# Optimization experiments

Hardware: AMD Instinct MI355X
Metric: run time of the kernel (lower is better)

The kernel has to match this reference:

```python
import jax, jax.numpy as jnp
import numpy as np

TOP_P = 0.9  # forward default arg, fixed to exercise the top-p path


def setup_inputs() -> dict:
    key = jax.random.key(0)
    k1, k2 = jax.random.split(key)
    B, V = 128, 128000
    logits = jax.random.normal(k1, (B, V), dtype=jnp.float32) * 2.0
    # temperatures in [0.5, 1.5) to avoid divide-by-near-zero
    temperatures = jax.random.uniform(k2, (B,), dtype=jnp.float32, minval=0.5, maxval=1.5)
    return {"logits": logits, "temperatures": temperatures, "top_k": 50}


def reference(logits, temperatures, top_k):
    B, V = logits.shape
    neg_inf = jnp.float32(-jnp.inf)

    # temperature scale + softmax
    scaled = logits.astype(jnp.float32) / temperatures[:, None]
    probs = jax.nn.softmax(scaled, axis=-1)  # (B, V)

    brow = jnp.arange(B)[:, None]

    # top-k filter: keep top-k probs, fill rest with -inf (matches torch scatter into full(-inf))
    if top_k > 0:
        k = min(top_k, V)
        vals, idx = jax.lax.top_k(probs, k)  # (B, k)
        probs = jnp.full_like(probs, neg_inf).at[brow, idx].set(vals)

    # top-p (nucleus) filter: sort desc, cumsum, mask tail beyond top_p (always keep first)
    if TOP_P < 1.0:
        order = jnp.argsort(-probs, axis=-1)              # descending order indices (-inf sorts last)
        sorted_probs = jnp.take_along_axis(probs, order, axis=-1)
        cum = jnp.cumsum(sorted_probs, axis=-1)
        remove = cum > TOP_P
        remove = remove.at[:, 0].set(False)
        sorted_probs = jnp.where(remove, neg_inf, sorted_probs)
        probs = probs.at[brow, order].set(sorted_probs)   # scatter back to original positions

    # Gumbel-max-style sampling: argmax(probs / Exp(1) noise), noise clamped to >= 1e-10
    kn = jax.random.fold_in(jax.random.key(0), 1)
    noise = jnp.maximum(jax.random.exponential(kn, probs.shape, dtype=jnp.float32), 1e-10)
    return jnp.argmax(probs / noise, axis=-1)  # (B,) int tokens
```

## Files before the change

### kernel.cpp

```cpp
#include <hip/hip_runtime.h>
#include <stdint.h>
#include <limits.h>

#define THREEFRY_PARTITIONABLE 1

#define NTK   512
#define NWAVE (NTK/64)
#define NBUCK 4096
#define BPT   (NBUCK/NTK)
#define CAPS  256
#define CAPG  2048
#define CAPF  512
#define KMAX  512
#define SMAX  32
#define CHUNK_TARGET 16384

#define NT1   1024
#define CAP1  4096

#if __has_builtin(__builtin_amdgcn_exp2f)
#define FAST_EXP2(x) __builtin_amdgcn_exp2f(x)
#else
#define FAST_EXP2(x) exp2f(x)
#endif

__device__ __forceinline__ uint32_t rotl32(uint32_t v, int r) {
  return (v << r) | (v >> (32 - r));
}
__device__ __forceinline__ void tfround(uint32_t& x0, uint32_t& x1, int r) {
  x0 += x1; x1 = rotl32(x1, r); x1 ^= x0;
}
__device__ __forceinline__ void threefry2x32(uint32_t k0, uint32_t k1,
                                             uint32_t x0, uint32_t x1,
                                             uint32_t& o0, uint32_t& o1) {
  uint32_t k2 = k0 ^ k1 ^ 0x1BD11BDAu;
  x0 += k0; x1 += k1;
  tfround(x0,x1,13); tfround(x0,x1,15); tfround(x0,x1,26); tfround(x0,x1,6);
  x0 += k1; x1 += k2 + 1u;
  tfround(x0,x1,17); tfround(x0,x1,29); tfround(x0,x1,16); tfround(x0,x1,24);
  x0 += k2; x1 += k0 + 2u;
  tfround(x0,x1,13); tfround(x0,x1,15); tfround(x0,x1,26); tfround(x0,x1,6);
  x0 += k0; x1 += k1 + 3u;
  tfround(x0,x1,17); tfround(x0,x1,29); tfround(x0,x1,16); tfround(x0,x1,24);
  x0 += k1; x1 += k2 + 4u;
  tfround(x0,x1,13); tfround(x0,x1,15); tfround(x0,x1,26); tfround(x0,x1,6);
  x0 += k2; x1 += k0 + 5u;
  o0 = x0; o1 = x1;
}
__device__ __forceinline__ float jax_noise(uint32_t kn0, uint32_t kn1,
                                           unsigned long long i,
                                           unsigned long long total) {
  uint32_t o0, o1, bits;
#if THREEFRY_PARTITIONABLE
  threefry2x32(kn0, kn1, (uint32_t)(i >> 32), (uint32_t)(i & 0xFFFFFFFFull), o0, o1);
  bits = o0 ^ o1;
#else
  unsigned long long H = total >> 1;
  if (i < H) { threefry2x32(kn0, kn1, (uint32_t)i, (uint32_t)(i + H), o0, o1); bits = o0; }
  else       { threefry2x32(kn0, kn1, (uint32_t)(i - H), (uint32_t)i, o0, o1); bits = o1; }
#endif
  float u = __uint_as_float((bits >> 9) | 0x3f800000u) - 1.0f;
  float e = -log1pf(-u);
  return fmaxf(e, 1e-10f);
}
__device__ __forceinline__ uint32_t fkey(float f) {
  uint32_t u = __float_as_uint(f);
  return u ^ ((u >> 31) ? 0xFFFFFFFFu : 0x80000000u);
}
__device__ __forceinline__ float unfkey_floor(uint32_t keyT) {
  if (keyT == 0u) return -INFINITY;
  return __uint_as_float((keyT & 0x80000000u) ? (keyT ^ 0x80000000u) : ~keyT);
}
__device__ __forceinline__ int clamp_k(int k) {
  if (k < 1) k = 1;
  if (k > KMAX) k = KMAX;
  return k;
}

__device__ __forceinline__ void block_kth_bucket(uint32_t* hist, uint32_t* wtot,
                                                 int* beta_sh, int k,
                                                 int tid, int lane, int wave) {
  const int base = tid * BPT;
  uint32_t tsum = 0;
#pragma unroll
  for (int j = 0; j < BPT; j++) tsum += hist[base + j];
  uint32_t incl = tsum;
  for (int off = 1; off < 64; off <<= 1) {
    uint32_t v = __shfl_down(incl, off);
    if (lane + off < 64) incl += v;
  }
  if (lane == 0) wtot[wave] = incl;
  __syncthreads();
  uint32_t above = incl - tsum;
  for (int w = wave + 1; w < NWAVE; w++) above += wtot[w];
  if (above < (uint32_t)k && above + tsum >= (uint32_t)k) {
    uint32_t run = above;
    for (int j = BPT - 1; j >= 0; j--) {
      run += hist[base + j];
      if (run >= (uint32_t)k) { *beta_sh = base + j; break; }
    }
  }
  __syncthreads();
}

__global__ __launch_bounds__(NTK)
void sampler_stream(const float* __restrict__ logits,
                    const float* __restrict__ temps,
                    const int* __restrict__ topk_ptr,
                    float* __restrict__ msArr,
                    double* __restrict__ dsumArr,
                    int* __restrict__ cntArr,
                    float2* __restrict__ pairs,
                    int B, int V, int S, int chunk) {
  const int blk = blockIdx.x;
  const int b = blk / S, sp = blk % S;
  const int tid = threadIdx.x, lane = tid & 63, wave = tid >> 6;

  __shared__ uint32_t hist[NBUCK];
  __shared__ float wm[NWAVE];
  __shared__ double wsum[NWAVE];
  __shared__ uint32_t wtot[NWAVE];
  __shared__ int beta_sh, cnum_sh;

  if (tid == 0) { beta_sh = 0; cnum_sh = 0; }
  for (int i = tid; i < NBUCK; i += NTK) hist[i] = 0;

  const float T = temps[b];
  const float cf = (float)(1.4426950408889634 / (double)T);
  const int k = clamp_k(*topk_ptr);

  const int start = sp * chunk;
  const int end = min(start + chunk, V);
  const float* row = logits + (size_t)b * (size_t)V;
  const int n = (end > start) ? (end - start) : 0;
  const int n4 = n >> 2;
  const float4* row4 = (const float4*)(row + start);

  float v0 = -INFINITY, v1 = -INFINITY;
  int   i0 = 0, i1 = 0;
  float acc0 = 0.f, acc1 = 0.f;

  auto proc = [&](float f, int idx) {
    bool gt0 = f > v0;
    bool gt1 = f > v1;
    float nv1 = gt0 ? v0 : (gt1 ? f : v1);
    int   ni1 = gt0 ? i0 : (gt1 ? idx : i1);
    v1 = nv1; i1 = ni1;
    v0 = gt0 ? f : v0;
    i0 = gt0 ? idx : i0;
  };
  auto proc4 = [&](float4 f, int vb) {
    proc(f.x, vb); proc(f.y, vb + 1); proc(f.z, vb + 2); proc(f.w, vb + 3);
    acc0 += FAST_EXP2(f.x * cf) + FAST_EXP2(f.z * cf);
    acc1 += FAST_EXP2(f.y * cf) + FAST_EXP2(f.w * cf);
  };

  int i = tid;
  for (; i + 3 * NTK < n4; i += 4 * NTK) {
    float4 fa = row4[i];
    float4 fb = row4[i + NTK];
    float4 fc = row4[i + 2 * NTK];
    float4 fd = row4[i + 3 * NTK];
    proc4(fa, start + i * 4);
    proc4(fb, start + (i + NTK) * 4);
    proc4(fc, start + (i + 2 * NTK) * 4);
    proc4(fd, start + (i + 3 * NTK) * 4);
  }
  for (; i < n4; i += NTK) {
    float4 fa = row4[i];
    proc4(fa, start + i * 4);
  }
  for (int v = start + n4 * 4 + tid; v < end; v += NTK) {
    float f = row[v];
    proc(f, v);
    acc0 += FAST_EXP2(f * cf);
  }

  float bm = v0;
  for (int off = 32; off; off >>= 1)
    bm = fmaxf(bm, __shfl_down(bm, off));
  if (lane == 0) wm[wave] = bm;

  double ds = (double)acc0 + (double)acc1;
  for (int off = 32; off; off >>= 1)
    ds += __shfl_down(ds, off);
  if (lane == 0) wsum[wave] = ds;

  if (v0 != -INFINITY) atomicAdd(&hist[fkey(v0) >> 20], 1u);
  __syncthreads();

  if (tid == 0) {
    float m_sp = wm[0];
#pragma unroll
    for (int w = 1; w < NWAVE; w++) m_sp = fmaxf(m_sp, wm[w]);
    msArr[blk] = m_sp;
    double t = 0.0;
    for (int w = 0; w < NWAVE; w++) t += wsum[w];
    dsumArr[blk] = t;
  }

  block_kth_bucket(hist, wtot, &beta_sh, k, tid, lane, wave);

  const float fT = unfkey_floor((uint32_t)beta_sh << 20);
  float2* myp = pairs + (size_t)blk * CAPS;

  if (v0 >= fT) {
    if (v1 >= fT) {
      for (int i2 = tid; i2 < n4; i2 += NTK) {
        float4 f = row4[i2];
        const int vb = start + i2 * 4;
        if (f.x >= fT) { int p = atomicAdd(&cnum_sh, 1); if (p < CAPS) myp[p] = make_float2(f.x, __int_as_float(vb)); }
        if (f.y >= fT) { int p = atomicAdd(&cnum_sh, 1); if (p < CAPS) myp[p] = make_float2(f.y, __int_as_float(vb + 1)); }
        if (f.z >= fT) { int p = atomicAdd(&cnum_sh, 1); if (p < CAPS) myp[p] = make_float2(f.z, __int_as_float(vb + 2)); }
        if (f.w >= fT) { int p = atomicAdd(&cnum_sh, 1); if (p < CAPS) myp[p] = make_float2(f.w, __int_as_float(vb + 3)); }
      }
      for (int v = start + n4 * 4 + tid; v < end; v += NTK) {
        float f = row[v];
        if (f >= fT) { int p = atomicAdd(&cnum_sh, 1); if (p < CAPS) myp[p] = make_float2(f, __int_as_float(v)); }
      }
    } else {
      int p = atomicAdd(&cnum_sh, 1);
      if (p < CAPS) myp[p] = make_float2(v0, __int_as_float(i0));
    }
  }
  __syncthreads();
  if (tid == 0) cntArr[blk] = min(cnum_sh, CAPS);
}

__global__ __launch_bounds__(NTK)
void sampler_finalize(const float* __restrict__ temps,
                      const int* __restrict__ topk_ptr,
                      const float* __restrict__ msArr,
                      const double* __restrict__ dsumArr,
                      const int* __restrict__ cntArr,
                      const float2* __restrict__ pairs,
                      int* __restrict__ out,
                      int B, int V, int S) {
  const int b = blockIdx.x;
  const int tid = threadIdx.x, lane = tid & 63, wave = tid >> 6;

  __shared__ uint32_t hist[NBUCK];
  __shared__ float gv[CAPG];
  __shared__ int   gi[CAPG];
  __shared__ float c2v[CAPF];
  __shared__ int   c2i[CAPF];
  __shared__ float c2p[CAPF];
  __shared__ float sv[KMAX];
  __shared__ int   si[KMAX];
  __shared__ float sc[KMAX];
  __shared__ int   offL[SMAX + 1];
  __shared__ int   cnL[SMAX];
  __shared__ float msL[SMAX];
  __shared__ double dsL[SMAX];
  __shared__ uint32_t wtot[NWAVE];
  __shared__ int beta_sh, cnt2_sh, L_sh;
  __shared__ float m_sh, D_sh;

  const int k = clamp_k(*topk_ptr);
  const float T = temps[b];

  if (tid == 0) { beta_sh = 0; cnt2_sh = 0; }
  if (tid < S) {
    msL[tid] = msArr[b * S + tid];
    dsL[tid] = dsumArr[b * S + tid];
    int c = cntArr[b * S + tid];
    cnL[tid] = (c < CAPS) ? c : CAPS;
  }
  for (int i = tid; i < NBUCK; i += NTK) hist[i] = 0;
  __syncthreads();

  if (tid == 0) {
    int acc = 0;
    for (int j = 0; j < S; j++) { offL[j] = acc; acc += cnL[j]; }
    offL[S] = acc;
  }

  if (wave == 1 || (NWAVE == 1 && wave == 0)) {
    float msp = (lane < S) ? msL[lane] : -INFINITY;
    float mg = msp;
    for (int off = 32; off; off >>= 1)
      mg = fmaxf(mg, __shfl_down(mg, off));
    mg = __shfl(mg, 0);
    double term = (lane < S) ? dsL[lane] : 0.0;
    for (int off = 32; off; off >>= 1)
      term += __shfl_down(term, off);
    if (lane == 0) {
      const double cd = 1.4426950408889634 / (double)T;
      D_sh = (float)(term * exp2(-(double)mg * cd));
      m_sh = mg / T;
    }
  }
  __syncthreads();

  const int TC = min(offL[S], CAPG);

  for (int t = tid; t < TC; t += NTK) {
    int j = 0;
#pragma unroll
    for (int jj = 1; jj <= SMAX; jj++)
      if (jj <= S) j += (t >= offL[jj]);
    float2 pr = pairs[(size_t)(b * S + j) * CAPS + (t - offL[j])];
    gv[t] = pr.x;
    gi[t] = __float_as_int(pr.y);
    atomicAdd(&hist[fkey(pr.x) >> 20], 1u);
  }
  __syncthreads();

  block_kth_bucket(hist, wtot, &beta_sh, k, tid, lane, wave);

  const float fT = unfkey_floor((uint32_t)beta_sh << 20);
  for (int t = tid; t < TC; t += NTK) {
    float val = gv[t];
    if (val >= fT) {
      int pos = atomicAdd(&cnt2_sh, 1);
      if (pos < CAPF) { c2v[pos] = val; c2i[pos] = gi[t]; }
    }
  }
  __syncthreads();

  const int C = min(cnt2_sh, CAPF);
  const float m = m_sh, D = D_sh;
  for (int i = tid; i < C; i += NTK)
    c2p[i] = expf(c2v[i] / T - m) / D;
  __syncthreads();

  for (int i = tid; i < C; i += NTK) {
    float pi = c2p[i];
    int   ii = c2i[i];
    int r = 0;
    for (int j = 0; j < C; j++) {
      float pj = c2p[j];
      r += (pj > pi) || (pj == pi && c2i[j] < ii);
    }
    if (r < k) { sv[r] = pi; si[r] = ii; }
  }
  __syncthreads();

  const int kk = (k < C) ? k : C;
  if (tid == 0) {
    float cum = 0.f;
    int L = 1;
    for (int j = 0; j < kk; j++) {
      cum += sv[j];
      if (j == 0) continue;
      if (cum <= 0.9f) L = j + 1; else break;
    }
    L_sh = L;
  }
  __syncthreads();

  const int L = L_sh;
  {
    uint32_t kn0, kn1;
    threefry2x32(0u, 0u, 0u, 1u, kn0, kn1);
    unsigned long long total = (unsigned long long)B * (unsigned long long)V;
    for (int j = tid; j < L; j += NTK) {
      unsigned long long flat = (unsigned long long)b * (unsigned long long)V
                              + (unsigned long long)si[j];
      sc[j] = sv[j] / jax_noise(kn0, kn1, flat, total);
    }
  }
  __syncthreads();

  if (tid == 0) {
    float bs = -1.0f;
    int   bi = INT_MAX;
    for (int j = 0; j < L; j++) {
      if (sc[j] > bs || (sc[j] == bs && si[j] < bi)) { bs = sc[j]; bi = si[j]; }
    }
    out[b] = bi;
  }
}

__global__ __launch_bounds__(NT1, 1)
void sampler_fallback(const float* __restrict__ logits,
                      const float* __restrict__ temps,
                      const int* __restrict__ topk_ptr,
                      int* __restrict__ out,
                      int B, int V) {
  const int b    = blockIdx.x;
  const int tid  = threadIdx.x;
  const int lane = tid & 63;
  const int wave = tid >> 6;

  __shared__ uint32_t hist[NBUCK];
  __shared__ float    cand_p[CAP1];
  __shared__ int      cand_i[CAP1];
  __shared__ float    wmax[16];
  __shared__ double   wsum[16];
  __shared__ float    svals[KMAX];
  __shared__ int      sidx[KMAX];
  __shared__ float    m_sh, D_sh;
  __shared__ int      beta_sh, cnum_sh, L_sh;

  const float T = temps[b];
  const float* row = logits + (size_t)b * (size_t)V;
  int k = clamp_k(*topk_ptr);
  if (k > V) k = V;

  if (tid == 0) { beta_sh = 1; cnum_sh = 0; }
  for (int i = tid; i < NBUCK; i += NT1) hist[i] = 0;
  __syncthreads();

  float t8[8];
#pragma unroll
  for (int j = 0; j < 8; j++) t8[j] = -INFINITY;
  float mymax = -INFINITY;
  for (int v = tid; v < V; v += NT1) {
    float s = row[v] / T;
    mymax = fmaxf(mymax, s);
    if (s > t8[0]) {
      t8[0] = s;
#pragma unroll
      for (int j = 1; j < 8; j++)
        if (t8[j-1] > t8[j]) { float tmp = t8[j]; t8[j] = t8[j-1]; t8[j-1] = tmp; }
    }
  }
  for (int off = 32; off > 0; off >>= 1)
    mymax = fmaxf(mymax, __shfl_down(mymax, off));
  if (lane == 0) wmax[wave] = mymax;
#pragma unroll
  for (int j = 0; j < 8; j++)
    if (t8[j] != -INFINITY) atomicAdd(&hist[fkey(t8[j]) >> 20], 1u);
  __syncthreads();
  if (tid == 0) {
    float m = -INFINITY;
    for (int w = 0; w < 16; w++) m = fmaxf(m, wmax[w]);
    m_sh = m;
  }
  if (wave == 1) {
    int base = lane * 64;
    uint32_t ssum = 0;
    for (int j = 0; j < 64; j++) ssum += hist[base + ((j + lane) & 63)];
    uint32_t incl = ssum;
    for (int off = 1; off < 64; off <<= 1) {
      uint32_t vv = __shfl_down(incl, off);
      if (lane + off < 64) incl += vv;
    }
    uint32_t higher = incl - ssum;
    if (higher < (uint32_t)k && incl >= (uint32_t)k) {
      uint32_t run = higher;
      for (int j = 63; j >= 0; j--) {
        run += hist[base + j];
        if (run >= (uint32_t)k) { beta_sh = base + j; break; }
      }
    }
  }
  __syncthreads();
  const float m = m_sh;
  const uint32_t keyT = (uint32_t)((beta_sh >= 1 ? beta_sh - 1 : 0)) << 20;
  double dsum = 0.0;
  for (int v = tid; v < V; v += NT1) {
    float s = row[v] / T;
    float e = expf(s - m);
    dsum += (double)e;
    if (fkey(s) >= keyT) {
      int pos = atomicAdd(&cnum_sh, 1);
      if (pos < CAP1) { cand_p[pos] = e; cand_i[pos] = v; }
    }
  }
  for (int off = 32; off > 0; off >>= 1)
    dsum += __shfl_down(dsum, off);
  if (lane == 0) wsum[wave] = dsum;
  __syncthreads();
  if (tid == 0) {
    double t = 0.0;
    for (int w = 0; w < 16; w++) t += wsum[w];
    D_sh = (float)t;
  }
  __syncthreads();
  const float D = D_sh;
  const int C = (cnum_sh < CAP1) ? cnum_sh : CAP1;
  for (int i = tid; i < C; i += NT1) cand_p[i] = cand_p[i] / D;
  __syncthreads();
  for (int i = tid; i < C; i += NT1) {
    float pi = cand_p[i];
    int   ii = cand_i[i];
    int r = 0;
    for (int j = 0; j < C; j++) {
      float pj = cand_p[j];
      r += (pj > pi) || (pj == pi && cand_i[j] < ii);
    }
    if (r < k) { svals[r] = pi; sidx[r] = ii; }
  }
  __syncthreads();
  if (tid == 0) {
    float cum = 0.f;
    int L = 1;
    for (int j = 0; j < k; j++) {
      cum += svals[j];
      if (j == 0) continue;
      if (cum <= 0.9f) L = j + 1; else break;
    }
    L_sh = L;
  }
  __syncthreads();
  const int L = L_sh;
  if (tid < L) {
    uint32_t kn0, kn1;
    threefry2x32(0u, 0u, 0u, 1u, kn0, kn1);
    unsigned long long total = (unsigned long long)B * (unsigned long long)V;
    unsigned long long flat = (unsigned long long)b * (unsigned long long)V
                            + (unsigned long long)sidx[tid];
    cand_p[tid] = svals[tid] / jax_noise(kn0, kn1, flat, total);
  }
  __syncthreads();
  if (tid == 0) {
    float bs = -1.0f;
    int   bi = INT_MAX;
    for (int j = 0; j < L; j++) {
      if (cand_p[j] > bs || (cand_p[j] == bs && sidx[j] < bi)) { bs = cand_p[j]; bi = sidx[j]; }
    }
    out[b] = bi;
  }
}

extern "C" void kernel_launch(void* const* d_in, const int* in_sizes, int n_in,
                              void* d_out, int out_size, void* d_ws, size_t ws_size,
                              hipStream_t stream) {
  const float* logits = (const float*)d_in[0];
  const float* temps  = (const float*)d_in[1];
  const int*   topk   = (const int*)d_in[2];
  int* out = (int*)d_out;

  int B = in_sizes[1];
  int V = in_sizes[0] / B;

  int S = (V + CHUNK_TARGET - 1) / CHUNK_TARGET;
  if (S > SMAX) S = SMAX;
  if (S < 1) S = 1;
  size_t need;
  for (;;) {
    need = (size_t)B * S * (sizeof(double) + sizeof(float) + sizeof(int))
         + (size_t)B * S * CAPS * sizeof(float2);
    if (need <= ws_size || S <= 2) break;
    S >>= 1;
  }

  if (ws_size < need || S < 2) {
    sampler_fallback<<<dim3(B), dim3(NT1), 0, stream>>>(logits, temps, topk, out, B, V);
    return;
  }

  int chunk = (((V + S - 1) / S) + 3) & ~3;

  double* dsumArr = (double*)d_ws;
  float*  msArr   = (float*)(dsumArr + (size_t)B * S);
  int*    cntArr  = (int*)(msArr + (size_t)B * S);
  float2* pairs   = (float2*)(cntArr + (size_t)B * S);

  sampler_stream<<<dim3(B * S), dim3(NTK), 0, stream>>>(
      logits, temps, topk, msArr, dsumArr, cntArr, pairs, B, V, S, chunk);
  sampler_finalize<<<dim3(B), dim3(NTK), 0, stream>>>(
      temps, topk, msArr, dsumArr, cntArr, pairs, out, B, V, S);
}
```

Measured before the change: 118.5 us.

## Fuse split-row stream and finalize kernels into one block-per-row sampler

```diff
diff --git a/kernel.cpp b/kernel.cpp
--- a/kernel.cpp
+++ b/kernel.cpp
@@ -4,19 +4,12 @@
 
 #define THREEFRY_PARTITIONABLE 1
 
-#define NTK   512
+#define NTK   1024
 #define NWAVE (NTK/64)
 #define NBUCK 4096
 #define BPT   (NBUCK/NTK)
-#define CAPS  256
-#define CAPG  2048
-#define CAPF  512
+#define CAP   2048
 #define KMAX  512
-#define SMAX  32
-#define CHUNK_TARGET 16384
-
-#define NT1   1024
-#define CAP1  4096
 
 #if __has_builtin(__builtin_amdgcn_exp2f)
 #define FAST_EXP2(x) __builtin_amdgcn_exp2f(x)
@@ -103,42 +96,42 @@
   __syncthreads();
 }
 
-__global__ __launch_bounds__(NTK)
-void sampler_stream(const float* __restrict__ logits,
-                    const float* __restrict__ temps,
-                    const int* __restrict__ topk_ptr,
-                    float* __restrict__ msArr,
-                    double* __restrict__ dsumArr,
-                    int* __restrict__ cntArr,
-                    float2* __restrict__ pairs,
-                    int B, int V, int S, int chunk) {
-  const int blk = blockIdx.x;
-  const int b = blk / S, sp = blk % S;
+__global__ __launch_bounds__(NTK, 1)
+void sampler_fused(const float* __restrict__ logits,
+                   const float* __restrict__ temps,
+                   const int* __restrict__ topk_ptr,
+                   int* __restrict__ out,
+                   int B, int V) {
+  const int b = blockIdx.x;
   const int tid = threadIdx.x, lane = tid & 63, wave = tid >> 6;
 
   __shared__ uint32_t hist[NBUCK];
+  __shared__ float cv[CAP];
+  __shared__ int   ci[CAP];
+  __shared__ float cp[CAP];
+  __shared__ float sv[KMAX];
+  __shared__ int   si[KMAX];
+  __shared__ float sc[KMAX];
   __shared__ float wm[NWAVE];
   __shared__ double wsum[NWAVE];
   __shared__ uint32_t wtot[NWAVE];
-  __shared__ int beta_sh, cnum_sh;
+  __shared__ int beta_sh, cnum_sh, L_sh;
+  __shared__ float m_sh, D_sh;
 
   if (tid == 0) { beta_sh = 0; cnum_sh = 0; }
   for (int i = tid; i < NBUCK; i += NTK) hist[i] = 0;
+  __syncthreads();
 
   const float T = temps[b];
   const float cf = (float)(1.4426950408889634 / (double)T);
   const int k = clamp_k(*topk_ptr);
-
-  const int start = sp * chunk;
-  const int end = min(start + chunk, V);
   const float* row = logits + (size_t)b * (size_t)V;
-  const int n = (end > start) ? (end - start) : 0;
-  const int n4 = n >> 2;
-  const float4* row4 = (const float4*)(row + start);
+  const int n4 = ((V & 3) == 0) ? (V >> 2) : 0;
+  const float4* row4 = (const float4*)row;
 
   float v0 = -INFINITY, v1 = -INFINITY;
   int   i0 = 0, i1 = 0;
-  float acc0 = 0.f, acc1 = 0.f;
+  float a0 = 0.f, a1 = 0.f, a2 = 0.f, a3 = 0.f;
 
   auto proc = [&](float f, int idx) {
     bool gt0 = f > v0;
@@ -149,10 +142,10 @@
     v0 = gt0 ? f : v0;
     i0 = gt0 ? idx : i0;
   };
-  auto proc4 = [&](float4 f, int vb) {
+  auto proc4 = [&](float4 f, int vb, float& a) {
     proc(f.x, vb); proc(f.y, vb + 1); proc(f.z, vb + 2); proc(f.w, vb + 3);
-    acc0 += FAST_EXP2(f.x * cf) + FAST_EXP2(f.z * cf);
-    acc1 += FAST_EXP2(f.y * cf) + FAST_EXP2(f.w * cf);
+    a += (FAST_EXP2(f.x * cf) + FAST_EXP2(f.y * cf))
+       + (FAST_EXP2(f.z * cf) + FAST_EXP2(f.w * cf));
   };
 
   int i = tid;
@@ -161,19 +154,19 @@
     float4 fb = row4[i + NTK];
     float4 fc = row4[i + 2 * NTK];
     float4 fd = row4[i + 3 * NTK];
-    proc4(fa, start + i * 4);
-    proc4(fb, start + (i + NTK) * 4);
-    proc4(fc, start + (i + 2 * NTK) * 4);
-    proc4(fd, start + (i + 3 * NTK) * 4);
+    proc4(fa, i * 4, a0);
+    proc4(fb, (i + NTK) * 4, a1);
+    proc4(fc, (i + 2 * NTK) * 4, a2);
+    proc4(fd, (i + 3 * NTK) * 4, a3);
   }
   for (; i < n4; i += NTK) {
     float4 fa = row4[i];
-    proc4(fa, start + i * 4);
-  }
-  for (int v = start + n4 * 4 + tid; v < end; v += NTK) {
+    proc4(fa, i * 4, a0);
+  }
+  for (int v = n4 * 4 + tid; v < V; v += NTK) {
     float f = row[v];
     proc(f, v);
-    acc0 += FAST_EXP2(f * cf);
+    a0 += FAST_EXP2(f * cf);
   }
 
   float bm = v0;
@@ -181,156 +174,61 @@
     bm = fmaxf(bm, __shfl_down(bm, off));
   if (lane == 0) wm[wave] = bm;
 
-  double ds = (double)acc0 + (double)acc1;
+  double ds = ((double)a0 + (double)a1) + ((double)a2 + (double)a3);
   for (int off = 32; off; off >>= 1)
     ds += __shfl_down(ds, off);
   if (lane == 0) wsum[wave] = ds;
 
   if (v0 != -INFINITY) atomicAdd(&hist[fkey(v0) >> 20], 1u);
+  if (v1 != -INFINITY) atomicAdd(&hist[fkey(v1) >> 20], 1u);
   __syncthreads();
 
   if (tid == 0) {
-    float m_sp = wm[0];
+    float mg = wm[0];
 #pragma unroll
-    for (int w = 1; w < NWAVE; w++) m_sp = fmaxf(m_sp, wm[w]);
-    msArr[blk] = m_sp;
+    for (int w = 1; w < NWAVE; w++) mg = fmaxf(mg, wm[w]);
     double t = 0.0;
     for (int w = 0; w < NWAVE; w++) t += wsum[w];
-    dsumArr[blk] = t;
+    const double cd = 1.4426950408889634 / (double)T;
+    D_sh = (float)(t * exp2(-(double)mg * cd));
+    m_sh = mg / T;
   }
 
   block_kth_bucket(hist, wtot, &beta_sh, k, tid, lane, wave);
 
   const float fT = unfkey_floor((uint32_t)beta_sh << 20);
-  float2* myp = pairs + (size_t)blk * CAPS;
-
-  if (v0 >= fT) {
-    if (v1 >= fT) {
-      for (int i2 = tid; i2 < n4; i2 += NTK) {
-        float4 f = row4[i2];
-        const int vb = start + i2 * 4;
-        if (f.x >= fT) { int p = atomicAdd(&cnum_sh, 1); if (p < CAPS) myp[p] = make_float2(f.x, __int_as_float(vb)); }
-        if (f.y >= fT) { int p = atomicAdd(&cnum_sh, 1); if (p < CAPS) myp[p] = make_float2(f.y, __int_as_float(vb + 1)); }
-        if (f.z >= fT) { int p = atomicAdd(&cnum_sh, 1); if (p < CAPS) myp[p] = make_float2(f.z, __int_as_float(vb + 2)); }
-        if (f.w >= fT) { int p = atomicAdd(&cnum_sh, 1); if (p < CAPS) myp[p] = make_float2(f.w, __int_as_float(vb + 3)); }
-      }
-      for (int v = start + n4 * 4 + tid; v < end; v += NTK) {
-        float f = row[v];
-        if (f >= fT) { int p = atomicAdd(&cnum_sh, 1); if (p < CAPS) myp[p] = make_float2(f, __int_as_float(v)); }
-      }
-    } else {
-      int p = atomicAdd(&cnum_sh, 1);
-      if (p < CAPS) myp[p] = make_float2(v0, __int_as_float(i0));
-    }
-  }
-  __syncthreads();
-  if (tid == 0) cntArr[blk] = min(cnum_sh, CAPS);
-}
-
-__global__ __launch_bounds__(NTK)
-void sampler_finalize(const float* __restrict__ temps,
-                      const int* __restrict__ topk_ptr,
-                      const float* __restrict__ msArr,
-                      const double* __restrict__ dsumArr,
-                      const int* __restrict__ cntArr,
-                      const float2* __restrict__ pairs,
-                      int* __restrict__ out,
-                      int B, int V, int S) {
-  const int b = blockIdx.x;
-  const int tid = threadIdx.x, lane = tid & 63, wave = tid >> 6;
-
-  __shared__ uint32_t hist[NBUCK];
-  __shared__ float gv[CAPG];
-  __shared__ int   gi[CAPG];
-  __shared__ float c2v[CAPF];
-  __shared__ int   c2i[CAPF];
-  __shared__ float c2p[CAPF];
-  __shared__ float sv[KMAX];
-  __shared__ int   si[KMAX];
-  __shared__ float sc[KMAX];
-  __shared__ int   offL[SMAX + 1];
-  __shared__ int   cnL[SMAX];
-  __shared__ float msL[SMAX];
-  __shared__ double dsL[SMAX];
-  __shared__ uint32_t wtot[NWAVE];
-  __shared__ int beta_sh, cnt2_sh, L_sh;
-  __shared__ float m_sh, D_sh;
-
-  const int k = clamp_k(*topk_ptr);
-  const float T = temps[b];
-
-  if (tid == 0) { beta_sh = 0; cnt2_sh = 0; }
-  if (tid < S) {
-    msL[tid] = msArr[b * S + tid];
-    dsL[tid] = dsumArr[b * S + tid];
-    int c = cntArr[b * S + tid];
-    cnL[tid] = (c < CAPS) ? c : CAPS;
-  }
-  for (int i = tid; i < NBUCK; i += NTK) hist[i] = 0;
-  __syncthreads();
-
-  if (tid == 0) {
-    int acc = 0;
-    for (int j = 0; j < S; j++) { offL[j] = acc; acc += cnL[j]; }
-    offL[S] = acc;
-  }
-
-  if (wave == 1 || (NWAVE == 1 && wave == 0)) {
-    float msp = (lane < S) ? msL[lane] : -INFINITY;
-    float mg = msp;
-    for (int off = 32; off; off >>= 1)
-      mg = fmaxf(mg, __shfl_down(mg, off));
-    mg = __shfl(mg, 0);
-    double term = (lane < S) ? dsL[lane] : 0.0;
-    for (int off = 32; off; off >>= 1)
-      term += __shfl_down(term, off);
-    if (lane == 0) {
-      const double cd = 1.4426950408889634 / (double)T;
-      D_sh = (float)(term * exp2(-(double)mg * cd));
-      m_sh = mg / T;
-    }
-  }
-  __syncthreads();
-
-  const int TC = min(offL[S], CAPG);
-
-  for (int t = tid; t < TC; t += NTK) {
-    int j = 0;
-#pragma unroll
-    for (int jj = 1; jj <= SMAX; jj++)
-      if (jj <= S) j += (t >= offL[jj]);
-    float2 pr = pairs[(size_t)(b * S + j) * CAPS + (t - offL[j])];
-    gv[t] = pr.x;
-    gi[t] = __float_as_int(pr.y);
-    atomicAdd(&hist[fkey(pr.x) >> 20], 1u);
-  }
-  __syncthreads();
-
-  block_kth_bucket(hist, wtot, &beta_sh, k, tid, lane, wave);
-
-  const float fT = unfkey_floor((uint32_t)beta_sh << 20);
-  for (int t = tid; t < TC; t += NTK) {
-    float val = gv[t];
-    if (val >= fT) {
-      int pos = atomicAdd(&cnt2_sh, 1);
-      if (pos < CAPF) { c2v[pos] = val; c2i[pos] = gi[t]; }
-    }
-  }
-  __syncthreads();
-
-  const int C = min(cnt2_sh, CAPF);
+  if (v1 >= fT) {
+    for (int i2 = tid; i2 < n4; i2 += NTK) {
+      float4 f = row4[i2];
+      const int vb = i2 * 4;
+      if (f.x >= fT) { int p = atomicAdd(&cnum_sh, 1); if (p < CAP) { cv[p] = f.x; ci[p] = vb; } }
+      if (f.y >= fT) { int p = atomicAdd(&cnum_sh, 1); if (p < CAP) { cv[p] = f.y; ci[p] = vb + 1; } }
+      if (f.z >= fT) { int p = atomicAdd(&cnum_sh, 1); if (p < CAP) { cv[p] = f.z; ci[p] = vb + 2; } }
+      if (f.w >= fT) { int p = atomicAdd(&cnum_sh, 1); if (p < CAP) { cv[p] = f.w; ci[p] = vb + 3; } }
+    }
+    for (int v = n4 * 4 + tid; v < V; v += NTK) {
+      float f = row[v];
+      if (f >= fT) { int p = atomicAdd(&cnum_sh, 1); if (p < CAP) { cv[p] = f; ci[p] = v; } }
+    }
+  } else if (v0 >= fT) {
+    int p = atomicAdd(&cnum_sh, 1);
+    if (p < CAP) { cv[p] = v0; ci[p] = i0; }
+  }
+  __syncthreads();
+
+  const int C = min(cnum_sh, CAP);
   const float m = m_sh, D = D_sh;
-  for (int i = tid; i < C; i += NTK)
-    c2p[i] = expf(c2v[i] / T - m) / D;
-  __syncthreads();
-
-  for (int i = tid; i < C; i += NTK) {
-    float pi = c2p[i];
-    int   ii = c2i[i];
+  for (int t = tid; t < C; t += NTK)
+    cp[t] = expf(cv[t] / T - m) / D;
+  __syncthreads();
+
+  for (int t = tid; t < C; t += NTK) {
+    float pi = cp[t];
+    int   ii = ci[t];
     int r = 0;
     for (int j = 0; j < C; j++) {
-      float pj = c2p[j];
-      r += (pj > pi) || (pj == pi && c2i[j] < ii);
+      float pj = cp[j];
+      r += (pj > pi) || (pj == pi && ci[j] < ii);
     }
     if (r < k) { sv[r] = pi; si[r] = ii; }
   }
@@ -372,149 +270,6 @@
   }
 }
 
-__global__ __launch_bounds__(NT1, 1)
-void sampler_fallback(const float* __restrict__ logits,
-                      const float* __restrict__ temps,
-                      const int* __restrict__ topk_ptr,
-                      int* __restrict__ out,
-                      int B, int V) {
-  const int b    = blockIdx.x;
-  const int tid  = threadIdx.x;
-  const int lane = tid & 63;
-  const int wave = tid >> 6;
-
-  __shared__ uint32_t hist[NBUCK];
-  __shared__ float    cand_p[CAP1];
-  __shared__ int      cand_i[CAP1];
-  __shared__ float    wmax[16];
-  __shared__ double   wsum[16];
-  __shared__ float    svals[KMAX];
-  __shared__ int      sidx[KMAX];
-  __shared__ float    m_sh, D_sh;
-  __shared__ int      beta_sh, cnum_sh, L_sh;
-
-  const float T = temps[b];
-  const float* row = logits + (size_t)b * (size_t)V;
-  int k = clamp_k(*topk_ptr);
-  if (k > V) k = V;
-
-  if (tid == 0) { beta_sh = 1; cnum_sh = 0; }
-  for (int i = tid; i < NBUCK; i += NT1) hist[i] = 0;
-  __syncthreads();
-
-  float t8[8];
-#pragma unroll
-  for (int j = 0; j < 8; j++) t8[j] = -INFINITY;
-  float mymax = -INFINITY;
-  for (int v = tid; v < V; v += NT1) {
-    float s = row[v] / T;
-    mymax = fmaxf(mymax, s);
-    if (s > t8[0]) {
-      t8[0] = s;
-#pragma unroll
-      for (int j = 1; j < 8; j++)
-        if (t8[j-1] > t8[j]) { float tmp = t8[j]; t8[j] = t8[j-1]; t8[j-1] = tmp; }
-    }
-  }
-  for (int off = 32; off > 0; off >>= 1)
-    mymax = fmaxf(mymax, __shfl_down(mymax, off));
-  if (lane == 0) wmax[wave] = mymax;
-#pragma unroll
-  for (int j = 0; j < 8; j++)
-    if (t8[j] != -INFINITY) atomicAdd(&hist[fkey(t8[j]) >> 20], 1u);
-  __syncthreads();
-  if (tid == 0) {
-    float m = -INFINITY;
-    for (int w = 0; w < 16; w++) m = fmaxf(m, wmax[w]);
-    m_sh = m;
-  }
-  if (wave == 1) {
-    int base = lane * 64;
-    uint32_t ssum = 0;
-    for (int j = 0; j < 64; j++) ssum += hist[base + ((j + lane) & 63)];
-    uint32_t incl = ssum;
-    for (int off = 1; off < 64; off <<= 1) {
-      uint32_t vv = __shfl_down(incl, off);
-      if (lane + off < 64) incl += vv;
-    }
-    uint32_t higher = incl - ssum;
-    if (higher < (uint32_t)k && incl >= (uint32_t)k) {
-      uint32_t run = higher;
-      for (int j = 63; j >= 0; j--) {
-        run += hist[base + j];
-        if (run >= (uint32_t)k) { beta_sh = base + j; break; }
-      }
-    }
-  }
-  __syncthreads();
-  const float m = m_sh;
-  const uint32_t keyT = (uint32_t)((beta_sh >= 1 ? beta_sh - 1 : 0)) << 20;
-  double dsum = 0.0;
-  for (int v = tid; v < V; v += NT1) {
-    float s = row[v] / T;
-    float e = expf(s - m);
-    dsum += (double)e;
-    if (fkey(s) >= keyT) {
-      int pos = atomicAdd(&cnum_sh, 1);
-      if (pos < CAP1) { cand_p[pos] = e; cand_i[pos] = v; }
-    }
-  }
-  for (int off = 32; off > 0; off >>= 1)
-    dsum += __shfl_down(dsum, off);
-  if (lane == 0) wsum[wave] = dsum;
-  __syncthreads();
-  if (tid == 0) {
-    double t = 0.0;
-    for (int w = 0; w < 16; w++) t += wsum[w];
-    D_sh = (float)t;
-  }
-  __syncthreads();
-  const float D = D_sh;
-  const int C = (cnum_sh < CAP1) ? cnum_sh : CAP1;
-  for (int i = tid; i < C; i += NT1) cand_p[i] = cand_p[i] / D;
-  __syncthreads();
-  for (int i = tid; i < C; i += NT1) {
-    float pi = cand_p[i];
-    int   ii = cand_i[i];
-    int r = 0;
-    for (int j = 0; j < C; j++) {
-      float pj = cand_p[j];
-      r += (pj > pi) || (pj == pi && cand_i[j] < ii);
-    }
-    if (r < k) { svals[r] = pi; sidx[r] = ii; }
-  }
-  __syncthreads();
-  if (tid == 0) {
-    float cum = 0.f;
-    int L = 1;
-    for (int j = 0; j < k; j++) {
-      cum += svals[j];
-      if (j == 0) continue;
-      if (cum <= 0.9f) L = j + 1; else break;
-    }
-    L_sh = L;
-  }
-  __syncthreads();
-  const int L = L_sh;
-  if (tid < L) {
-    uint32_t kn0, kn1;
-    threefry2x32(0u, 0u, 0u, 1u, kn0, kn1);
-    unsigned long long total = (unsigned long long)B * (unsigned long long)V;
-    unsigned long long flat = (unsigned long long)b * (unsigned long long)V
-                            + (unsigned long long)sidx[tid];
-    cand_p[tid] = svals[tid] / jax_noise(kn0, kn1, flat, total);
-  }
-  __syncthreads();
-  if (tid == 0) {
-    float bs = -1.0f;
-    int   bi = INT_MAX;
-    for (int j = 0; j < L; j++) {
-      if (cand_p[j] > bs || (cand_p[j] == bs && sidx[j] < bi)) { bs = cand_p[j]; bi = sidx[j]; }
-    }
-    out[b] = bi;
-  }
-}
-
 extern "C" void kernel_launch(void* const* d_in, const int* in_sizes, int n_in,
                               void* d_out, int out_size, void* d_ws, size_t ws_size,
                               hipStream_t stream) {
@@ -526,31 +281,5 @@
   int B = in_sizes[1];
   int V = in_sizes[0] / B;
 
-  int S = (V + CHUNK_TARGET - 1) / CHUNK_TARGET;
-  if (S > SMAX) S = SMAX;
-  if (S < 1) S = 1;
-  size_t need;
-  for (;;) {
-    need = (size_t)B * S * (sizeof(double) + sizeof(float) + sizeof(int))
-         + (size_t)B * S * CAPS * sizeof(float2);
-    if (need <= ws_size || S <= 2) break;
-    S >>= 1;
-  }
-
-  if (ws_size < need || S < 2) {
-    sampler_fallback<<<dim3(B), dim3(NT1), 0, stream>>>(logits, temps, topk, out, B, V);
-    return;
-  }
-
-  int chunk = (((V + S - 1) / S) + 3) & ~3;
-
-  double* dsumArr = (double*)d_ws;
-  float*  msArr   = (float*)(dsumArr + (size_t)B * S);
-  int*    cntArr  = (int*)(msArr + (size_t)B * S);
-  float2* pairs   = (float2*)(cntArr + (size_t)B * S);
-
-  sampler_stream<<<dim3(B * S), dim3(NTK), 0, stream>>>(
-      logits, temps, topk, msArr, dsumArr, cntArr, pairs, B, V, S, chunk);
-  sampler_finalize<<<dim3(B), dim3(NTK), 0, stream>>>(
-      temps, topk, msArr, dsumArr, cntArr, pairs, out, B, V, S);
-}
+  sampler_fused<<<dim3(B), dim3(NTK), 0, stream>>>(logits, temps, topk, out, B, V);
+}
```

Result: faster. 115.1 us (-2.9%).
